# Kernel optimization log

Hardware: AMD Instinct MI355X
Metric: run time of the kernel (lower is better)

## Reference

```python
import jax, jax.numpy as jnp
import numpy as np
import math

V, D, H, F, NL, C = 32000, 768, 12, 3072, 6, 10
DK = D // H
EPS = 1e-5


def sinusoidal_pe(L, d_model):
    pos = jnp.arange(L, dtype=jnp.float32)[:, None]
    div = jnp.exp(jnp.arange(0, d_model, 2, dtype=jnp.float32) * (-math.log(10000.0) / d_model))
    pe = jnp.zeros((L, d_model), dtype=jnp.float32)
    pe = pe.at[:, 0::2].set(jnp.sin(pos * div))
    pe = pe.at[:, 1::2].set(jnp.cos(pos * div))
    return pe


def layer_norm(x, g, b):
    mu = jnp.mean(x, axis=-1, keepdims=True)
    var = jnp.mean(jnp.square(x - mu), axis=-1, keepdims=True)
    return (x - mu) / jnp.sqrt(var + EPS) * g + b


def setup_inputs() -> dict:
    key = jax.random.key(0)
    ks = jax.random.split(key, 24)
    s = 0.02
    inp = {
        "input_ids": jax.random.randint(ks[0], (8, 1024), 0, V),
        "mask": jnp.ones((8, 1024), dtype=jnp.int32),
        "emb": jax.random.normal(ks[1], (V, D), dtype=jnp.float32) * s,
        "wq": jax.random.normal(ks[2], (NL, D, D), dtype=jnp.float32) * s,
        "bq": jnp.zeros((NL, D), dtype=jnp.float32),
        "wk": jax.random.normal(ks[3], (NL, D, D), dtype=jnp.float32) * s,
        "bk": jnp.zeros((NL, D), dtype=jnp.float32),
        "wv": jax.random.normal(ks[4], (NL, D, D), dtype=jnp.float32) * s,
        "bv": jnp.zeros((NL, D), dtype=jnp.float32),
        "wo": jax.random.normal(ks[5], (NL, D, D), dtype=jnp.float32) * s,
        "bo": jnp.zeros((NL, D), dtype=jnp.float32),
        "ln1_g": jnp.ones((NL, D), dtype=jnp.float32),
        "ln1_b": jnp.zeros((NL, D), dtype=jnp.float32),
        "w1": jax.random.normal(ks[6], (NL, D, F), dtype=jnp.float32) * s,
        "b1": jnp.zeros((NL, F), dtype=jnp.float32),
        "w2": jax.random.normal(ks[7], (NL, F, D), dtype=jnp.float32) * s,
        "b2": jnp.zeros((NL, D), dtype=jnp.float32),
        "ln2_g": jnp.ones((NL, D), dtype=jnp.float32),
        "ln2_b": jnp.zeros((NL, D), dtype=jnp.float32),
        "cls_w": jax.random.normal(ks[8], (D, C), dtype=jnp.float32) * s,
        "cls_b": jnp.zeros((C,), dtype=jnp.float32),
    }
    return inp


def reference(input_ids, mask, emb, wq, bq, wk, bk, wv, bv, wo, bo,
              ln1_g, ln1_b, w1, b1, w2, b2, ln2_g, ln2_b, cls_w, cls_b):
    B, L = input_ids.shape
    x = emb[input_ids] + sinusoidal_pe(L, D)[None, :, :]  # [B,L,D]
    # mask broadcast: [B,1,1,L] over key positions
    neg = jnp.where(mask[:, None, None, :] == 0, -1e9, 0.0).astype(x.dtype)

    def block(x, p):
        lwq, lbq, lwk, lbk, lwv, lbv, lwo, lbo, g1, bb1, lw1, lb1, lw2, lb2, g2, bb2 = p
        q = (x @ lwq + lbq).reshape(B, L, H, DK)
        k = (x @ lwk + lbk).reshape(B, L, H, DK)
        v = (x @ lwv + lbv).reshape(B, L, H, DK)
        scores = jnp.einsum("blhd,bmhd->bhlm", q, k) / math.sqrt(DK) + neg
        attn = jax.nn.softmax(scores, axis=-1)
        out = jnp.einsum("bhlm,bmhd->blhd", attn, v).reshape(B, L, D)
        out = out @ lwo + lbo
        x = layer_norm(x + out, g1, bb1)
        ff = jnp.maximum(x @ lw1 + lb1, 0.0) @ lw2 + lb2
        x = layer_norm(x + ff, g2, bb2)
        return x, None

    params = (wq, bq, wk, bk, wv, bv, wo, bo, ln1_g, ln1_b, w1, b1, w2, b2, ln2_g, ln2_b)
    x, _ = jax.lax.scan(block, x, params)
    return x[:, 0, :] @ cls_w + cls_b
```

## Files before the change

kernel.cpp:

```cpp
#include <hip/hip_runtime.h>
#include <stdint.h>

typedef unsigned short u16;
typedef __bf16 bf16x8 __attribute__((ext_vector_type(8)));
typedef float f32x4 __attribute__((ext_vector_type(4)));

#define NLAYER 6
#define DM 768
#define NH 12
#define FD 3072
#define NCLS 10
#define BATCH 8
#define SEQ 1024
#define NTOK (BATCH*SEQ)
#define PST 72

__device__ __forceinline__ u16 f2bf(float f) {
  union { float f; unsigned u; } v; v.f = f;
  unsigned u = v.u;
  return (u16)((u + 0x7fffu + ((u >> 16) & 1u)) >> 16);
}

__device__ __forceinline__ void async16(const void* g, void* l) {
  __builtin_amdgcn_global_load_lds(
      (__attribute__((address_space(1))) void*)(void*)g,
      (__attribute__((address_space(3))) void*)l, 16, 0, 0);
}

__global__ __launch_bounds__(256) void pack_weights(
    const float* __restrict__ src, u16* __restrict__ dst,
    int K, int N, long srcLS, long dstLS, int ntOff, int ntCount)
{
  int z = blockIdx.z;
  int K32 = K >> 5;
  int fid = blockIdx.x * 4 + (threadIdx.x >> 6);
  int ntL = fid / K32, kc = fid - ntL * K32;
  if (ntL >= ntCount) return;
  int lane = threadIdx.x & 63;
  int l15 = lane & 15, quad = lane >> 4;
  int n = ntL * 16 + l15;
  const float* s = src + (long)z * srcLS + (long)(kc * 32 + quad * 8) * N + n;
  unsigned pk[4];
  #pragma unroll
  for (int j = 0; j < 4; j++) {
    u16 a = f2bf(s[(2 * j) * (long)N]);
    u16 b = f2bf(s[(2 * j + 1) * (long)N]);
    pk[j] = (unsigned)a | ((unsigned)b << 16);
  }
  u16* d = dst + (long)z * dstLS + ((long)(ntOff + ntL) * K32 + kc) * 512 + lane * 8;
  *(uint4*)d = *(uint4*)pk;
}

__global__ void concat_bias(const float* __restrict__ bq, const float* __restrict__ bk,
                            const float* __restrict__ bv, float* __restrict__ qkvb)
{
  int i = blockIdx.x * 256 + threadIdx.x;
  if (i >= NLAYER * 2304) return;
  int layer = i / 2304, c = i % 2304;
  float v;
  if (c < 768) v = bq[layer * 768 + c];
  else if (c < 1536) v = bk[layer * 768 + c - 768];
  else v = bv[layer * 768 + c - 1536];
  qkvb[i] = v;
}

__global__ __launch_bounds__(256) void embed_kernel(
    const int* __restrict__ ids, const float* __restrict__ emb,
    float* __restrict__ x, u16* __restrict__ xb)
{
  int e = (blockIdx.x * 256 + threadIdx.x) * 4;
  int d = e % DM;
  int tok = e / DM;
  int l = tok % SEQ;
  int id = ids[tok];
  float4 em = *(const float4*)(emb + (long)id * DM + d);
  const float cexp = -9.210340371976184f / 768.f;
  float div0 = __expf((float)d * cexp);
  float div1 = __expf((float)(d + 2) * cexp);
  float a0 = (float)l * div0, a1 = (float)l * div1;
  em.x += sinf(a0); em.y += cosf(a0);
  em.z += sinf(a1); em.w += cosf(a1);
  *(float4*)(x + e) = em;
  uint2 pk;
  pk.x = f2bf(em.x) | ((unsigned)f2bf(em.y) << 16);
  pk.y = f2bf(em.z) | ((unsigned)f2bf(em.w) << 16);
  *(uint2*)(xb + e) = pk;
}

template<int TM>
__global__ __launch_bounds__(256) void gemm_pk(
    const u16* __restrict__ A, const u16* __restrict__ WP,
    const float* __restrict__ bias,
    float* __restrict__ Cf, u16* __restrict__ Cb, u16* __restrict__ VTout,
    int N, int K, int relu)
{
  constexpr int MI  = TM / 32;
  constexpr int ACH = TM / 8;
  constexpr int ASZ = (TM == 128) ? 9216 : TM * 64;
  __shared__ __align__(16) u16 As[ASZ];
  int tid = threadIdx.x;
  int wave = tid >> 6, lane = tid & 63;
  int wm = (wave >> 1) * (TM / 2);
  int wn = (wave & 1) * 64;
  int l15 = lane & 15, quad = lane >> 4;
  long mBase = (long)blockIdx.x * TM;
  long nBase = (long)blockIdx.y * 128;
  int K32 = K >> 5;
  int r8 = lane >> 3;
  int g8 = ((lane & 7) ^ r8) * 8;

  const u16* gsrc[ACH / 4];
  u16* ldst[ACH / 4];
  #pragma unroll
  for (int idx = 0; idx < ACH / 4; idx++) {
    int c = wave + idx * 4;
    gsrc[idx] = A + (mBase + c * 8 + r8) * (long)K + g8;
    ldst[idx] = As + c * 512;
  }
  int sw = l15 & 7;
  int aoff[2];
  #pragma unroll
  for (int kc = 0; kc < 2; kc++)
    aoff[kc] = (wm + l15) * 64 + 8 * ((kc * 4 + quad) ^ sw);

  const u16* bpp = WP + ((long)(nBase >> 4) + (wn >> 4)) * K32 * 512 + lane * 8;
  uint4 bnx[2][4];
  #pragma unroll
  for (int kc = 0; kc < 2; kc++)
    #pragma unroll
    for (int j = 0; j < 4; j++)
      bnx[kc][j] = *(const uint4*)(bpp + ((long)j * K32 + kc) * 512);

  f32x4 acc[MI][4] = {};

  for (int k0 = 0; k0 < K; k0 += 64) {
    __syncthreads();
    #pragma unroll
    for (int idx = 0; idx < ACH / 4; idx++)
      async16(gsrc[idx] + k0, ldst[idx]);
    __syncthreads();

    uint4 bcur[2][4];
    #pragma unroll
    for (int kc = 0; kc < 2; kc++)
      #pragma unroll
      for (int j = 0; j < 4; j++)
        bcur[kc][j] = bnx[kc][j];
    if (k0 + 64 < K) {
      int nch = (k0 >> 5) + 2;
      #pragma unroll
      for (int kc = 0; kc < 2; kc++)
        #pragma unroll
        for (int j = 0; j < 4; j++)
          bnx[kc][j] = *(const uint4*)(bpp + ((long)j * K32 + nch + kc) * 512);
    }
    #pragma unroll
    for (int kc = 0; kc < 2; kc++) {
      bf16x8 aF[MI];
      #pragma unroll
      for (int i = 0; i < MI; i++) aF[i] = *(const bf16x8*)(As + aoff[kc] + i * 1024);
      #pragma unroll
      for (int i = 0; i < MI; i++)
        #pragma unroll
        for (int j = 0; j < 4; j++) {
          bf16x8 bb = *(bf16x8*)&bcur[kc][j];
          acc[i][j] = __builtin_amdgcn_mfma_f32_16x16x32_bf16(aF[i], bb, acc[i][j], 0, 0, 0);
        }
    }
  }

  if (VTout != nullptr && nBase >= 1536) {
    #pragma unroll
    for (int j = 0; j < 4; j++) {
      long gn = nBase + wn + j * 16 + l15;
      float bv = bias[gn];
      int h = ((int)gn - 1536) >> 6, dk = (int)gn & 63;
      #pragma unroll
      for (int i = 0; i < MI; i++) {
        long gm0 = mBase + wm + i * 16 + quad * 4;
        int bb = (int)(gm0 >> 10), seq = (int)(gm0 & 1023);
        u16* dst = VTout + (((long)(bb * NH + h) * 64 + dk) << 10) + seq;
        uint2 pk;
        pk.x = f2bf(acc[i][j][0] + bv) | ((unsigned)f2bf(acc[i][j][1] + bv) << 16);
        pk.y = f2bf(acc[i][j][2] + bv) | ((unsigned)f2bf(acc[i][j][3] + bv) << 16);
        *(uint2*)dst = pk;
      }
    }
  } else if (Cb != nullptr) {
    if constexpr (TM == 128) {
      __syncthreads();
      u16* ep = As + wave * 2304;
      float bvj[4];
      #pragma unroll
      for (int j = 0; j < 4; j++) bvj[j] = bias[nBase + wn + j * 16 + l15];
      #pragma unroll
      for (int h = 0; h < 2; h++) {
        #pragma unroll
        for (int ii = 0; ii < 2; ii++) {
          int i = 2 * h + ii;
          #pragma unroll
          for (int j = 0; j < 4; j++)
            #pragma unroll
            for (int r = 0; r < 4; r++) {
              float v = acc[i][j][r] + bvj[j];
              if (relu) v = fmaxf(v, 0.f);
              ep[(ii * 16 + quad * 4 + r) * 72 + j * 16 + l15] = f2bf(v);
            }
        }
        #pragma unroll
        for (int rr = 0; rr < 2; rr++) {
          int row = (lane >> 2) + rr * 16;
          int c = (lane & 3) * 16;
          uint4 d0 = *(const uint4*)&ep[row * 72 + c];
          uint4 d1 = *(const uint4*)&ep[row * 72 + c + 8];
          long gm = mBase + wm + h * 32 + row;
          u16* dst = Cb + gm * (long)N + nBase + wn + c;
          *(uint4*)dst = d0;
          *(uint4*)(dst + 8) = d1;
        }
      }
    }
  } else {
    #pragma unroll
    for (int j = 0; j < 4; j++) {
      long gn = nBase + wn + j * 16 + l15;
      float bv = bias[gn];
      #pragma unroll
      for (int i = 0; i < MI; i++) {
        long gm0 = mBase + wm + i * 16 + quad * 4;
        #pragma unroll
        for (int r = 0; r < 4; r++) {
          float v = acc[i][j][r] + bv;
          if (relu) v = fmaxf(v, 0.f);
          Cf[(gm0 + r) * (long)N + gn] = v;
        }
      }
    }
  }
}

__global__ __launch_bounds__(256) void attention_mfma(
    const u16* __restrict__ qkvb, const int* __restrict__ mask,
    const u16* __restrict__ vtg, u16* __restrict__ ctxb)
{
  __shared__ __align__(16) u16 Kb[64 * 64];
  __shared__ __align__(16) u16 Vt[64 * 64];
  __shared__ __align__(16) u16 Pl[4][16 * PST];
  __shared__ float negs[64];
  int tid = threadIdx.x;
  int wave = tid >> 6, lane = tid & 63;
  int l15 = lane & 15, quad = lane >> 4;
  int qt = blockIdx.x, bh = blockIdx.y;
  int b = bh / NH, h = bh - b * NH;
  long qtok = (long)b * SEQ + qt * 64;

  bf16x8 aQ[2];
  {
    const u16* qp = qkvb + (qtok + wave * 16 + l15) * 2304 + h * 64 + quad * 8;
    aQ[0] = *(const bf16x8*)qp;
    aQ[1] = *(const bf16x8*)(qp + 32);
  }
  f32x4 oacc[4] = {};
  float lrow[4] = {0.f, 0.f, 0.f, 0.f};

  int r8 = lane >> 3;
  int g8 = ((lane & 7) ^ r8) * 8;
  int ck0 = wave * 2, ck1 = wave * 2 + 1;
  const u16* kg0 = qkvb + ((long)b * SEQ + ck0 * 8 + r8) * 2304 + 768 + h * 64 + g8;
  const u16* kg1 = qkvb + ((long)b * SEQ + ck1 * 8 + r8) * 2304 + 768 + h * 64 + g8;
  const u16* vg0 = vtg + ((long)bh * 64 + ck0 * 8 + r8) * SEQ + g8;
  const u16* vg1 = vtg + ((long)bh * 64 + ck1 * 8 + r8) * SEQ + g8;
  int sw = l15 & 7;
  int soff[2], aoffP[2];
  #pragma unroll
  for (int kc = 0; kc < 2; kc++) {
    soff[kc]  = l15 * 64 + 8 * ((kc * 4 + quad) ^ sw);
    aoffP[kc] = l15 * PST + kc * 32 + quad * 8;
  }
  u16* pw = &Pl[wave][0];

  for (int kt = 0; kt < 16; kt++) {
    __syncthreads();
    async16(kg0 + (long)kt * 64 * 2304, Kb + ck0 * 512);
    async16(kg1 + (long)kt * 64 * 2304, Kb + ck1 * 512);
    async16(vg0 + kt * 64, Vt + ck0 * 512);
    async16(vg1 + kt * 64, Vt + ck1 * 512);
    if (tid < 64) negs[tid] = (mask[(long)b * SEQ + kt * 64 + tid] == 0) ? -1e9f : 0.f;
    __syncthreads();

    f32x4 sa[4] = {};
    #pragma unroll
    for (int kc = 0; kc < 2; kc++)
      #pragma unroll
      for (int n = 0; n < 4; n++) {
        bf16x8 bk = *(const bf16x8*)&Kb[n * 1024 + soff[kc]];
        sa[n] = __builtin_amdgcn_mfma_f32_16x16x32_bf16(aQ[kc], bk, sa[n], 0, 0, 0);
      }
    float ng[4];
    #pragma unroll
    for (int n = 0; n < 4; n++) ng[n] = negs[n * 16 + l15];
    #pragma unroll
    for (int n = 0; n < 4; n++)
      #pragma unroll
      for (int r = 0; r < 4; r++) {
        float s = fminf(sa[n][r] * 0.125f + ng[n], 60.f);
        float p = __expf(s);
        lrow[r] += p;
        pw[(quad * 4 + r) * PST + n * 16 + l15] = f2bf(p);
      }
    #pragma unroll
    for (int kc = 0; kc < 2; kc++) {
      bf16x8 ap = *(const bf16x8*)&pw[aoffP[kc]];
      #pragma unroll
      for (int d = 0; d < 4; d++) {
        bf16x8 bv = *(const bf16x8*)&Vt[d * 1024 + soff[kc]];
        oacc[d] = __builtin_amdgcn_mfma_f32_16x16x32_bf16(ap, bv, oacc[d], 0, 0, 0);
      }
    }
  }

  #pragma unroll
  for (int r = 0; r < 4; r++) {
    lrow[r] += __shfl_xor(lrow[r], 1, 64);
    lrow[r] += __shfl_xor(lrow[r], 2, 64);
    lrow[r] += __shfl_xor(lrow[r], 4, 64);
    lrow[r] += __shfl_xor(lrow[r], 8, 64);
  }
  float inv[4];
  #pragma unroll
  for (int r = 0; r < 4; r++) inv[r] = 1.f / lrow[r];
  #pragma unroll
  for (int d = 0; d < 4; d++)
    #pragma unroll
    for (int r = 0; r < 4; r++)
      pw[(quad * 4 + r) * PST + d * 16 + l15] = f2bf(oacc[d][r] * inv[r]);
  int orow = lane >> 2, ocol = (lane & 3) * 16;
  u16* og = ctxb + (qtok + wave * 16 + orow) * DM + h * 64 + ocol;
  *(uint4*)og       = *(const uint4*)&pw[orow * PST + ocol];
  *(uint4*)(og + 8) = *(const uint4*)&pw[orow * PST + ocol + 8];
}

__global__ __launch_bounds__(64) void ln_residual(
    const float* __restrict__ x, const float* __restrict__ y,
    const float* __restrict__ g, const float* __restrict__ b,
    float* __restrict__ xout, u16* __restrict__ xbout)
{
  long row = blockIdx.x;
  int t = threadIdx.x;
  const float* xr = x + row * DM;
  const float* yr = y + row * DM;
  float v[12];
  float sum = 0.f, sq = 0.f;
  #pragma unroll
  for (int j = 0; j < 3; j++) {
    int d = j * 256 + t * 4;
    float4 a = *(const float4*)(xr + d);
    float4 c = *(const float4*)(yr + d);
    float z0 = a.x + c.x, z1 = a.y + c.y, z2 = a.z + c.z, z3 = a.w + c.w;
    v[j*4+0] = z0; v[j*4+1] = z1; v[j*4+2] = z2; v[j*4+3] = z3;
    sum += z0 + z1 + z2 + z3;
    sq  += z0*z0 + z1*z1 + z2*z2 + z3*z3;
  }
  #pragma unroll
  for (int m = 1; m < 64; m <<= 1) {
    sum += __shfl_xor(sum, m, 64);
    sq  += __shfl_xor(sq,  m, 64);
  }
  float mu = sum * (1.f / 768.f);
  float var = sq * (1.f / 768.f) - mu * mu;
  float rstd = rsqrtf(var + 1e-5f);
  #pragma unroll
  for (int j = 0; j < 3; j++) {
    int d = j * 256 + t * 4;
    float4 gg = *(const float4*)(g + d);
    float4 bb = *(const float4*)(b + d);
    float z0 = (v[j*4+0] - mu) * rstd * gg.x + bb.x;
    float z1 = (v[j*4+1] - mu) * rstd * gg.y + bb.y;
    float z2 = (v[j*4+2] - mu) * rstd * gg.z + bb.z;
    float z3 = (v[j*4+3] - mu) * rstd * gg.w + bb.w;
    float4 fz; fz.x = z0; fz.y = z1; fz.z = z2; fz.w = z3;
    *(float4*)(xout + row * DM + d) = fz;
    uint2 pk;
    pk.x = f2bf(z0) | ((unsigned)f2bf(z1) << 16);
    pk.y = f2bf(z2) | ((unsigned)f2bf(z3) << 16);
    *(uint2*)(xbout + row * DM + d) = pk;
  }
}

__global__ __launch_bounds__(64) void classifier_kernel(
    const float* __restrict__ x, const float* __restrict__ w,
    const float* __restrict__ bias, float* __restrict__ out)
{
  int bc = blockIdx.x;
  int b = bc / NCLS, c = bc % NCLS;
  const float* xr = x + (long)b * SEQ * DM;
  float sum = 0.f;
  for (int d = threadIdx.x; d < DM; d += 64)
    sum += xr[d] * w[d * NCLS + c];
  #pragma unroll
  for (int m = 1; m < 64; m <<= 1) sum += __shfl_xor(sum, m, 64);
  if (threadIdx.x == 0) out[bc] = sum + bias[c];
}

extern "C" void kernel_launch(void* const* d_in, const int* in_sizes, int n_in,
                              void* d_out, int out_size, void* d_ws, size_t ws_size,
                              hipStream_t stream)
{
  const int*   ids  = (const int*)d_in[0];
  const int*   mask = (const int*)d_in[1];
  const float* emb  = (const float*)d_in[2];
  const float* wq   = (const float*)d_in[3];
  const float* bq   = (const float*)d_in[4];
  const float* wk   = (const float*)d_in[5];
  const float* bk   = (const float*)d_in[6];
  const float* wv   = (const float*)d_in[7];
  const float* bv   = (const float*)d_in[8];
  const float* wo   = (const float*)d_in[9];
  const float* bo   = (const float*)d_in[10];
  const float* ln1g = (const float*)d_in[11];
  const float* ln1b = (const float*)d_in[12];
  const float* w1   = (const float*)d_in[13];
  const float* b1   = (const float*)d_in[14];
  const float* w2   = (const float*)d_in[15];
  const float* b2   = (const float*)d_in[16];
  const float* ln2g = (const float*)d_in[17];
  const float* ln2b = (const float*)d_in[18];
  const float* clsw = (const float*)d_in[19];
  const float* clsb = (const float*)d_in[20];

  char* ws = (char*)d_ws;
  size_t off = 0;
  auto alloc = [&](size_t bytes) -> void* {
    void* p = ws + off;
    off += (bytes + 255) & ~(size_t)255;
    return p;
  };
  float* X      = (float*)alloc((size_t)NTOK * DM * 4);
  u16*   XB     = (u16*)  alloc((size_t)NTOK * DM * 2);
  u16*   QKVB16 = (u16*)  alloc((size_t)NTOK * 2304 * 2);
  u16*   VT     = (u16*)  alloc((size_t)96 * 64 * SEQ * 2);
  u16*   CTXB   = (u16*)  alloc((size_t)NTOK * DM * 2);
  u16*   H1B    = (u16*)  alloc((size_t)NTOK * FD * 2);
  float* SCR    = (float*)alloc((size_t)NTOK * DM * 4);
  u16*   WQKV_P = (u16*)  alloc((size_t)NLAYER * 144 * 24 * 512 * 2);
  u16*   WO_P   = (u16*)  alloc((size_t)NLAYER * 48 * 24 * 512 * 2);
  u16*   W1_P   = (u16*)  alloc((size_t)NLAYER * 192 * 24 * 512 * 2);
  u16*   W2_P   = (u16*)  alloc((size_t)NLAYER * 48 * 96 * 512 * 2);
  float* QKVB   = (float*)alloc((size_t)NLAYER * 2304 * 4);

  const long LSW = 768L * 768;
  pack_weights<<<dim3(288, 1, 6), 256, 0, stream>>>(wq, WQKV_P, 768, 768, LSW, 144L*24*512, 0, 48);
  pack_weights<<<dim3(288, 1, 6), 256, 0, stream>>>(wk, WQKV_P, 768, 768, LSW, 144L*24*512, 48, 48);
  pack_weights<<<dim3(288, 1, 6), 256, 0, stream>>>(wv, WQKV_P, 768, 768, LSW, 144L*24*512, 96, 48);
  pack_weights<<<dim3(288, 1, 6), 256, 0, stream>>>(wo, WO_P, 768, 768, LSW, 48L*24*512, 0, 48);
  pack_weights<<<dim3(1152, 1, 6), 256, 0, stream>>>(w1, W1_P, 768, 3072, 768L*3072, 192L*24*512, 0, 192);
  pack_weights<<<dim3(1152, 1, 6), 256, 0, stream>>>(w2, W2_P, 3072, 768, 3072L*768, 48L*96*512, 0, 48);
  concat_bias<<<(NLAYER * 2304 + 255) / 256, 256, 0, stream>>>(bq, bk, bv, QKVB);
  embed_kernel<<<NTOK * DM / 1024, 256, 0, stream>>>(ids, emb, X, XB);

  for (int L = 0; L < NLAYER; L++) {
    gemm_pk<128><<<dim3(64, 18), 256, 0, stream>>>(
        XB, WQKV_P + (size_t)L * 144 * 24 * 512, QKVB + L * 2304,
        nullptr, QKVB16, VT, 2304, 768, 0);
    attention_mfma<<<dim3(16, 96), 256, 0, stream>>>(QKVB16, mask, VT, CTXB);
    gemm_pk<64><<<dim3(128, 6), 256, 0, stream>>>(
        CTXB, WO_P + (size_t)L * 48 * 24 * 512, bo + L * 768,
        SCR, nullptr, nullptr, 768, 768, 0);
    ln_residual<<<NTOK, 64, 0, stream>>>(X, SCR, ln1g + L * 768, ln1b + L * 768, X, XB);
    gemm_pk<128><<<dim3(64, 24), 256, 0, stream>>>(
        XB, W1_P + (size_t)L * 192 * 24 * 512, b1 + L * 3072,
        nullptr, H1B, nullptr, 3072, 768, 1);
    gemm_pk<64><<<dim3(128, 6), 256, 0, stream>>>(
        H1B, W2_P + (size_t)L * 48 * 96 * 512, b2 + L * 768,
        SCR, nullptr, nullptr, 768, 3072, 0);
    ln_residual<<<NTOK, 64, 0, stream>>>(X, SCR, ln2g + L * 768, ln2b + L * 768, X, XB);
  }
  classifier_kernel<<<80, 64, 0, stream>>>(X, clsw, clsb, (float*)d_out);
}
```

Measured before the change: 2.093 ms.

## Double-buffer GEMM A tiles, batch LayerNorm rows, shrink W2 GEMM tile

```diff
diff --git a/kernel.cpp b/kernel.cpp
--- a/kernel.cpp
+++ b/kernel.cpp
@@ -94,9 +94,11 @@
     float* __restrict__ Cf, u16* __restrict__ Cb, u16* __restrict__ VTout,
     int N, int K, int relu)
 {
-  constexpr int MI  = TM / 32;
-  constexpr int ACH = TM / 8;
-  constexpr int ASZ = (TM == 128) ? 9216 : TM * 64;
+  constexpr int MI    = TM / 32;
+  constexpr int ACH   = TM / 8;
+  constexpr int NAS   = (ACH + 3) / 4;
+  constexpr int BUFSZ = TM * 64;
+  constexpr int ASZ   = (2 * BUFSZ > 9216) ? 2 * BUFSZ : 9216;
   __shared__ __align__(16) u16 As[ASZ];
   int tid = threadIdx.x;
   int wave = tid >> 6, lane = tid & 63;
@@ -109,13 +111,13 @@
   int r8 = lane >> 3;
   int g8 = ((lane & 7) ^ r8) * 8;
 
-  const u16* gsrc[ACH / 4];
-  u16* ldst[ACH / 4];
-  #pragma unroll
-  for (int idx = 0; idx < ACH / 4; idx++) {
+  const u16* gsrc[NAS];
+  int choff[NAS];
+  #pragma unroll
+  for (int idx = 0; idx < NAS; idx++) {
     int c = wave + idx * 4;
     gsrc[idx] = A + (mBase + c * 8 + r8) * (long)K + g8;
-    ldst[idx] = As + c * 512;
+    choff[idx] = c * 512;
   }
   int sw = l15 & 7;
   int aoff[2];
@@ -124,6 +126,10 @@
     aoff[kc] = (wm + l15) * 64 + 8 * ((kc * 4 + quad) ^ sw);
 
   const u16* bpp = WP + ((long)(nBase >> 4) + (wn >> 4)) * K32 * 512 + lane * 8;
+
+  #pragma unroll
+  for (int idx = 0; idx < NAS; idx++)
+    async16(gsrc[idx], As + choff[idx]);
   uint4 bnx[2][4];
   #pragma unroll
   for (int kc = 0; kc < 2; kc++)
@@ -133,13 +139,16 @@
 
   f32x4 acc[MI][4] = {};
 
-  for (int k0 = 0; k0 < K; k0 += 64) {
+  int it = 0;
+  for (int k0 = 0; k0 < K; k0 += 64, it++) {
     __syncthreads();
-    #pragma unroll
-    for (int idx = 0; idx < ACH / 4; idx++)
-      async16(gsrc[idx] + k0, ldst[idx]);
-    __syncthreads();
-
+    const u16* buf = As + (it & 1) * BUFSZ;
+    if (k0 + 64 < K) {
+      u16* nb = As + ((it + 1) & 1) * BUFSZ;
+      #pragma unroll
+      for (int idx = 0; idx < NAS; idx++)
+        async16(gsrc[idx] + k0 + 64, nb + choff[idx]);
+    }
     uint4 bcur[2][4];
     #pragma unroll
     for (int kc = 0; kc < 2; kc++)
@@ -158,7 +167,7 @@
     for (int kc = 0; kc < 2; kc++) {
       bf16x8 aF[MI];
       #pragma unroll
-      for (int i = 0; i < MI; i++) aF[i] = *(const bf16x8*)(As + aoff[kc] + i * 1024);
+      for (int i = 0; i < MI; i++) aF[i] = *(const bf16x8*)(buf + aoff[kc] + i * 1024);
       #pragma unroll
       for (int i = 0; i < MI; i++)
         #pragma unroll
@@ -340,13 +349,13 @@
   *(uint4*)(og + 8) = *(const uint4*)&pw[orow * PST + ocol + 8];
 }
 
-__global__ __launch_bounds__(64) void ln_residual(
+__global__ __launch_bounds__(256) void ln_residual(
     const float* __restrict__ x, const float* __restrict__ y,
     const float* __restrict__ g, const float* __restrict__ b,
     float* __restrict__ xout, u16* __restrict__ xbout)
 {
-  long row = blockIdx.x;
-  int t = threadIdx.x;
+  long row = blockIdx.x * 4 + (threadIdx.x >> 6);
+  int t = threadIdx.x & 63;
   const float* xr = x + row * DM;
   const float* yr = y + row * DM;
   float v[12];
@@ -466,14 +475,14 @@
     gemm_pk<64><<<dim3(128, 6), 256, 0, stream>>>(
         CTXB, WO_P + (size_t)L * 48 * 24 * 512, bo + L * 768,
         SCR, nullptr, nullptr, 768, 768, 0);
-    ln_residual<<<NTOK, 64, 0, stream>>>(X, SCR, ln1g + L * 768, ln1b + L * 768, X, XB);
+    ln_residual<<<NTOK / 4, 256, 0, stream>>>(X, SCR, ln1g + L * 768, ln1b + L * 768, X, XB);
     gemm_pk<128><<<dim3(64, 24), 256, 0, stream>>>(
         XB, W1_P + (size_t)L * 192 * 24 * 512, b1 + L * 3072,
         nullptr, H1B, nullptr, 3072, 768, 1);
-    gemm_pk<64><<<dim3(128, 6), 256, 0, stream>>>(
+    gemm_pk<32><<<dim3(256, 6), 256, 0, stream>>>(
         H1B, W2_P + (size_t)L * 48 * 96 * 512, b2 + L * 768,
         SCR, nullptr, nullptr, 768, 3072, 0);
-    ln_residual<<<NTOK, 64, 0, stream>>>(X, SCR, ln2g + L * 768, ln2b + L * 768, X, XB);
+    ln_residual<<<NTOK / 4, 256, 0, stream>>>(X, SCR, ln2g + L * 768, ln2b + L * 768, X, XB);
   }
   classifier_kernel<<<80, 64, 0, stream>>>(X, clsw, clsb, (float*)d_out);
 }
```

Result: slower. 2.284 ms (+9.1%).
